# Kernel tuning notes

Hardware: AMD Instinct MI355X
Metric: run time of the kernel (lower is better)

## Reference

```python
import jax, jax.numpy as jnp
import numpy as np

B, T, D, H, STEPS = 4096, 128, 4, 64, 60


def setup_inputs() -> dict:
    key = jax.random.key(0)
    ks = jax.random.split(key, 12)
    s = 0.1
    return {
        "x": jax.random.normal(ks[0], (B, T, D), dtype=jnp.float32),
        # layer 0 (input size D)
        "Wih0": jax.random.normal(ks[1], (4 * H, D), dtype=jnp.float32) * s,
        "Whh0": jax.random.normal(ks[2], (4 * H, H), dtype=jnp.float32) * s,
        "bih0": jax.random.normal(ks[3], (4 * H,), dtype=jnp.float32) * s,
        "bhh0": jax.random.normal(ks[4], (4 * H,), dtype=jnp.float32) * s,
        # layer 1 (input size H)
        "Wih1": jax.random.normal(ks[5], (4 * H, H), dtype=jnp.float32) * s,
        "Whh1": jax.random.normal(ks[6], (4 * H, H), dtype=jnp.float32) * s,
        "bih1": jax.random.normal(ks[7], (4 * H,), dtype=jnp.float32) * s,
        "bhh1": jax.random.normal(ks[8], (4 * H,), dtype=jnp.float32) * s,
        # output head
        "Wfc": jax.random.normal(ks[9], (D, H), dtype=jnp.float32) * s,
        "bfc": jax.random.normal(ks[10], (D,), dtype=jnp.float32) * s,
    }


def _lstm_cell(h, c, x, Wih, Whh, bih, bhh):
    # PyTorch gate order: i, f, g, o
    gates = x @ Wih.T + h @ Whh.T + (bih + bhh)  # [B, 4H]
    i, f, g, o = jnp.split(gates, 4, axis=-1)
    c_new = jax.nn.sigmoid(f) * c + jax.nn.sigmoid(i) * jnp.tanh(g)
    h_new = jax.nn.sigmoid(o) * jnp.tanh(c_new)
    return h_new, c_new


def reference(x, Wih0, Whh0, bih0, bhh0, Wih1, Whh1, bih1, bhh1, Wfc, bfc):
    b = x.shape[0]
    zeros = jnp.zeros((b, H), dtype=x.dtype)

    def two_layer(carry, xt):
        h0, c0, h1, c1 = carry
        h0, c0 = _lstm_cell(h0, c0, xt, Wih0, Whh0, bih0, bhh0)
        h1, c1 = _lstm_cell(h1, c1, h0, Wih1, Whh1, bih1, bhh1)
        return (h0, c0, h1, c1), h1

    # encode history: scan over time (xs: [T, B, D])
    carry0 = (zeros, zeros, zeros, zeros)
    carry, _ = jax.lax.scan(two_layer, carry0, jnp.swapaxes(x, 0, 1))

    def ar_step(state, _):
        carry, cur = state
        carry, h1 = two_layer(carry, cur)
        pred = h1 @ Wfc.T + bfc  # [B, D]
        return (carry, pred), pred

    _, preds = jax.lax.scan(ar_step, (carry, x[:, -1, :]), None, length=STEPS)
    return jnp.swapaxes(preds, 0, 1)  # [B, STEPS, D]
```

## Files before the change

kernel.cpp:

```cpp
#include <hip/hip_runtime.h>


#define T_ENC 128
#define D_IN 4
#define H 64
#define STEPS 60
#define M 16
#define A0S 104
#define A1S 136

typedef _Float16 half8 __attribute__((ext_vector_type(8)));
typedef _Float16 half4_t __attribute__((ext_vector_type(4)));
typedef float float4v __attribute__((ext_vector_type(4)));

__device__ __forceinline__ float fast_sigmoid(float x) {
    float e = __builtin_amdgcn_exp2f(-1.44269504f * x);
    return __builtin_amdgcn_rcpf(1.0f + e);
}
__device__ __forceinline__ float fast_tanh(float x) {
    float e = __builtin_amdgcn_exp2f(2.88539008f * x);
    return __builtin_fmaf(-2.0f, __builtin_amdgcn_rcpf(e + 1.0f), 1.0f);
}

__global__ __launch_bounds__(256, 1) void lstm_ar_kernel(
    const float* __restrict__ x,
    const float* __restrict__ Wih0, const float* __restrict__ Whh0,
    const float* __restrict__ bih0, const float* __restrict__ bhh0,
    const float* __restrict__ Wih1, const float* __restrict__ Whh1,
    const float* __restrict__ bih1, const float* __restrict__ bhh1,
    const float* __restrict__ Wfc,  const float* __restrict__ bfc,
    float* __restrict__ out)
{
    __shared__ __align__(16) _Float16 A0buf[2][M * A0S];
    __shared__ __align__(16) _Float16 A1buf[2][M * A1S];
    __shared__ __align__(16) float    xstash[2][512];
    __shared__ __align__(16) float    predsS[M * STEPS * D_IN];

    const int tid  = threadIdx.x;
    const int wave = tid >> 6;
    const int lane = tid & 63;
    const int n16  = lane & 15;
    const int quad = lane >> 4;
    const int m0   = blockIdx.x * M;
    const int m    = n16;
    const int jcol = 16 * wave + n16;

    { _Float16* z = &A0buf[0][0]; for (int i = tid; i < 2 * M * A0S; i += 256) z[i] = (_Float16)0.f; }
    { _Float16* z = &A1buf[0][0]; for (int i = tid; i < 2 * M * A1S; i += 256) z[i] = (_Float16)0.f; }

    half8 B0f[3][4];
    half8 B1f[4][4];
    half8 B0ar[4][4];
    half8 Bfc[2];
    float b0v[4], b1v[4], b0ar[4];
    #pragma unroll
    for (int tau = 0; tau < 4; ++tau) {
        const int n = 16 * (wave + 4 * tau) + n16;
        b0v[tau] = bih0[n] + bhh0[n];
        b1v[tau] = bih1[n] + bhh1[n];
        float wb = 0.f;
        #pragma unroll
        for (int d = 0; d < 4; ++d) wb += Wih0[n * D_IN + d] * bfc[d];
        b0ar[tau] = b0v[tau] + wb;
        #pragma unroll
        for (int kt = 0; kt < 3; ++kt)
            #pragma unroll
            for (int j = 0; j < 8; ++j) {
                const int k = kt * 32 + quad * 8 + j;
                float v = 0.f;
                if (k < 4)       v = Wih0[n * D_IN + k];
                else if (k < 68) v = Whh0[n * H + (k - 4)];
                B0f[kt][tau][j] = (_Float16)v;
            }
        #pragma unroll
        for (int kt = 0; kt < 4; ++kt)
            #pragma unroll
            for (int j = 0; j < 8; ++j) {
                const int k = kt * 32 + quad * 8 + j;
                const float v = (k < H) ? Wih1[n * H + k] : Whh1[n * H + (k - H)];
                B1f[kt][tau][j] = (_Float16)v;
            }
        #pragma unroll
        for (int kt = 0; kt < 4; ++kt)
            #pragma unroll
            for (int j = 0; j < 8; ++j) {
                const int k = kt * 32 + quad * 8 + j;
                float v;
                if (k < H) v = Whh0[n * H + k];
                else {
                    const int c = k - H;
                    v = Wih0[n * D_IN + 0] * Wfc[0 * H + c] + Wih0[n * D_IN + 1] * Wfc[1 * H + c]
                      + Wih0[n * D_IN + 2] * Wfc[2 * H + c] + Wih0[n * D_IN + 3] * Wfc[3 * H + c];
                }
                B0ar[kt][tau][j] = (_Float16)v;
            }
    }
    float bfcv = 0.f;
    if (wave == 0) {
        #pragma unroll
        for (int kt = 0; kt < 2; ++kt)
            #pragma unroll
            for (int j = 0; j < 8; ++j) {
                const int k = kt * 32 + quad * 8 + j;
                Bfc[kt][j] = (_Float16)((n16 < 4) ? Wfc[n16 * H + k] : 0.f);
            }
        if (n16 < 4) bfcv = bfc[n16];
    }

    float c0s[4] = {0.f, 0.f, 0.f, 0.f};
    float c1s[4] = {0.f, 0.f, 0.f, 0.f};

    __syncthreads();

    if (wave == 2) {
        const int elem = lane >> 2, st2 = (lane & 3) * 2;
        const float4v xa = *(const float4v*)&x[((size_t)(m0 + elem) * T_ENC + st2) * 4];
        const float4v xb = *(const float4v*)&x[((size_t)(m0 + elem) * T_ENC + st2 + 1) * 4];
        *(float4v*)&xstash[0][elem * 32 + st2 * 4]       = xa;
        *(float4v*)&xstash[0][elem * 32 + (st2 + 1) * 4] = xb;
    }
    __syncthreads();
    if (wave == 2 && lane < 16) {
        const float4v v0 = *(const float4v*)&xstash[0][lane * 32 + 0];
        const float4v v1 = *(const float4v*)&xstash[0][lane * 32 + 4];
        *(half4_t*)&A0buf[1][lane * A0S] =
            (half4_t){(_Float16)v0[0], (_Float16)v0[1], (_Float16)v0[2], (_Float16)v0[3]};
        *(half4_t*)&A0buf[0][lane * A0S] =
            (half4_t){(_Float16)v1[0], (_Float16)v1[1], (_Float16)v1[2], (_Float16)v1[3]};
    }
    __syncthreads();

    {
        half8 a0f[3];
        #pragma unroll
        for (int kt = 0; kt < 3; ++kt)
            a0f[kt] = *(const half8*)&A0buf[1][m * A0S + kt * 32 + quad * 8];
        float4v C0[4];
        #pragma unroll
        for (int tau = 0; tau < 4; ++tau)
            C0[tau] = (float4v){b0v[tau], b0v[tau], b0v[tau], b0v[tau]};
        #pragma unroll
        for (int kt = 0; kt < 3; ++kt)
            #pragma unroll
            for (int tau = 0; tau < 4; ++tau)
                C0[tau] = __builtin_amdgcn_mfma_f32_16x16x32_f16(a0f[kt], B0f[kt][tau], C0[tau], 0, 0, 0);
        #pragma unroll
        for (int r = 0; r < 4; ++r) {
            const float ig = fast_sigmoid(C0[0][r]);
            const float fg = fast_sigmoid(C0[1][r]);
            const float gg = fast_tanh   (C0[2][r]);
            const float og = fast_sigmoid(C0[3][r]);
            const float c  = fg * c0s[r] + ig * gg;
            c0s[r] = c;
            const _Float16 hh = (_Float16)(og * fast_tanh(c));
            const int row = quad * 4 + r;
            A1buf[0][row * A1S + jcol]     = hh;
            A0buf[0][row * A0S + 4 + jcol] = hh;
        }
    }
    __syncthreads();

    float4v xpa, xpb;

    for (int t = 0; t < T_ENC; ++t) {
        const int p = t & 1;
        const _Float16* cur0 = &A0buf[p][0];
        const _Float16* cur1 = &A1buf[p][0];
        _Float16* nxt0 = &A0buf[1 - p][0];
        _Float16* nxt1 = &A1buf[1 - p][0];

        if (wave == 2) {
            if ((t & 7) == 0) {
                const int k = (t >> 3) + 1;
                const int elem = lane >> 2, st2 = (lane & 3) * 2;
                int t1 = 8 * k + st2;     if (t1 > 127) t1 = 127;
                int t2 = 8 * k + st2 + 1; if (t2 > 127) t2 = 127;
                xpa = *(const float4v*)&x[((size_t)(m0 + elem) * T_ENC + t1) * 4];
                xpb = *(const float4v*)&x[((size_t)(m0 + elem) * T_ENC + t2) * 4];
            }
            if ((t & 7) == 4) {
                const int bf = ((t >> 3) + 1) & 1;
                const int elem = lane >> 2, st2 = (lane & 3) * 2;
                *(float4v*)&xstash[bf][elem * 32 + st2 * 4]       = xpa;
                *(float4v*)&xstash[bf][elem * 32 + (st2 + 1) * 4] = xpb;
            }
        }

        half8 a1f[4], a0f[3];
        #pragma unroll
        for (int kt = 0; kt < 4; ++kt)
            a1f[kt] = *(const half8*)&cur1[m * A1S + kt * 32 + quad * 8];
        #pragma unroll
        for (int kt = 0; kt < 3; ++kt)
            a0f[kt] = *(const half8*)&cur0[m * A0S + kt * 32 + quad * 8];

        float4v C1[4], C0[4];
        #pragma unroll
        for (int tau = 0; tau < 4; ++tau) {
            C1[tau] = (float4v){b1v[tau], b1v[tau], b1v[tau], b1v[tau]};
            C0[tau] = (float4v){b0v[tau], b0v[tau], b0v[tau], b0v[tau]};
        }
        #pragma unroll
        for (int kt = 0; kt < 4; ++kt)
            #pragma unroll
            for (int tau = 0; tau < 4; ++tau)
                C1[tau] = __builtin_amdgcn_mfma_f32_16x16x32_f16(a1f[kt], B1f[kt][tau], C1[tau], 0, 0, 0);
        #pragma unroll
        for (int kt = 0; kt < 3; ++kt)
            #pragma unroll
            for (int tau = 0; tau < 4; ++tau)
                C0[tau] = __builtin_amdgcn_mfma_f32_16x16x32_f16(a0f[kt], B0f[kt][tau], C0[tau], 0, 0, 0);

        #pragma unroll
        for (int r = 0; r < 4; ++r) {
            const float ig = fast_sigmoid(C1[0][r]);
            const float fg = fast_sigmoid(C1[1][r]);
            const float gg = fast_tanh   (C1[2][r]);
            const float og = fast_sigmoid(C1[3][r]);
            const float c  = fg * c1s[r] + ig * gg;
            c1s[r] = c;
            const int row = quad * 4 + r;
            nxt1[row * A1S + 64 + jcol] = (_Float16)(og * fast_tanh(c));
        }
        #pragma unroll
        for (int r = 0; r < 4; ++r) {
            const float ig = fast_sigmoid(C0[0][r]);
            const float fg = fast_sigmoid(C0[1][r]);
            const float gg = fast_tanh   (C0[2][r]);
            const float og = fast_sigmoid(C0[3][r]);
            const float c  = fg * c0s[r] + ig * gg;
            c0s[r] = c;
            const _Float16 hh = (_Float16)(og * fast_tanh(c));
            const int row = quad * 4 + r;
            nxt1[row * A1S + jcol]     = hh;
            nxt0[row * A0S + 4 + jcol] = hh;
        }
        if (wave == 2 && lane < 16) {
            const int st = (t + 2) & 7, bf = ((t + 2) >> 3) & 1;
            const float4v v = *(const float4v*)&xstash[bf][lane * 32 + st * 4];
            *(half4_t*)&nxt0[lane * A0S] =
                (half4_t){(_Float16)v[0], (_Float16)v[1], (_Float16)v[2], (_Float16)v[3]};
        }
        __syncthreads();
    }

    for (int s = 0; s < STEPS; ++s) {
        const int q = s & 1;
        const _Float16* cur = &A1buf[q][0];
        _Float16* nxt = &A1buf[1 - q][0];

        half8 a1f[4];
        #pragma unroll
        for (int kt = 0; kt < 4; ++kt)
            a1f[kt] = *(const half8*)&cur[m * A1S + kt * 32 + quad * 8];
        float4v C1[4];
        #pragma unroll
        for (int tau = 0; tau < 4; ++tau)
            C1[tau] = (float4v){b1v[tau], b1v[tau], b1v[tau], b1v[tau]};
        #pragma unroll
        for (int kt = 0; kt < 4; ++kt)
            #pragma unroll
            for (int tau = 0; tau < 4; ++tau)
                C1[tau] = __builtin_amdgcn_mfma_f32_16x16x32_f16(a1f[kt], B1f[kt][tau], C1[tau], 0, 0, 0);
        #pragma unroll
        for (int r = 0; r < 4; ++r) {
            const float ig = fast_sigmoid(C1[0][r]);
            const float fg = fast_sigmoid(C1[1][r]);
            const float gg = fast_tanh   (C1[2][r]);
            const float og = fast_sigmoid(C1[3][r]);
            const float c  = fg * c1s[r] + ig * gg;
            c1s[r] = c;
            const int row = quad * 4 + r;
            nxt[row * A1S + 64 + jcol] = (_Float16)(og * fast_tanh(c));
        }
        __syncthreads();

        half8 aA[4];
        #pragma unroll
        for (int kt = 0; kt < 2; ++kt)
            aA[kt] = *(const half8*)&cur[m * A1S + kt * 32 + quad * 8];
        #pragma unroll
        for (int kt = 2; kt < 4; ++kt)
            aA[kt] = *(const half8*)&nxt[m * A1S + 64 + (kt - 2) * 32 + quad * 8];
        float4v C0[4];
        #pragma unroll
        for (int tau = 0; tau < 4; ++tau)
            C0[tau] = (float4v){b0ar[tau], b0ar[tau], b0ar[tau], b0ar[tau]};
        #pragma unroll
        for (int kt = 0; kt < 4; ++kt)
            #pragma unroll
            for (int tau = 0; tau < 4; ++tau)
                C0[tau] = __builtin_amdgcn_mfma_f32_16x16x32_f16(aA[kt], B0ar[kt][tau], C0[tau], 0, 0, 0);

        if (wave == 0) {
            float4v Cp = (float4v){bfcv, bfcv, bfcv, bfcv};
            Cp = __builtin_amdgcn_mfma_f32_16x16x32_f16(aA[2], Bfc[0], Cp, 0, 0, 0);
            Cp = __builtin_amdgcn_mfma_f32_16x16x32_f16(aA[3], Bfc[1], Cp, 0, 0, 0);
            if (n16 < 4) {
                #pragma unroll
                for (int r = 0; r < 4; ++r)
                    predsS[(quad * 4 + r) * (STEPS * D_IN) + s * 4 + n16] = Cp[r];
            }
        }

        #pragma unroll
        for (int r = 0; r < 4; ++r) {
            const float ig = fast_sigmoid(C0[0][r]);
            const float fg = fast_sigmoid(C0[1][r]);
            const float gg = fast_tanh   (C0[2][r]);
            const float og = fast_sigmoid(C0[3][r]);
            const float c  = fg * c0s[r] + ig * gg;
            c0s[r] = c;
            const int row = quad * 4 + r;
            nxt[row * A1S + jcol] = (_Float16)(og * fast_tanh(c));
        }
        __syncthreads();
    }

    for (int j = tid; j < M * STEPS; j += 256) {
        const int elem = j / STEPS, r = j - elem * STEPS;
        ((float4v*)out)[(size_t)(m0 + elem) * STEPS + r] = ((const float4v*)predsS)[j];
    }
}

extern "C" void kernel_launch(void* const* d_in, const int* in_sizes, int n_in,
                              void* d_out, int out_size, void* d_ws, size_t ws_size,
                              hipStream_t stream) {
    const float* x    = (const float*)d_in[0];
    const float* Wih0 = (const float*)d_in[1];
    const float* Whh0 = (const float*)d_in[2];
    const float* bih0 = (const float*)d_in[3];
    const float* bhh0 = (const float*)d_in[4];
    const float* Wih1 = (const float*)d_in[5];
    const float* Whh1 = (const float*)d_in[6];
    const float* bih1 = (const float*)d_in[7];
    const float* bhh1 = (const float*)d_in[8];
    const float* Wfc  = (const float*)d_in[9];
    const float* bfc  = (const float*)d_in[10];
    float* out = (float*)d_out;

    dim3 grid(4096 / M);
    dim3 block(256);
    lstm_ar_kernel<<<grid, block, 0, stream>>>(
        x, Wih0, Whh0, bih0, bhh0, Wih1, Whh1, bih1, bhh1, Wfc, bfc, out);
}
```

Baseline: 308.2 us.

## Split LSTM layers across two wave groups with 512-thread blocks

Doubles the block to 512 threads so one group of four waves runs layer 1 while the other runs layer 0, in parallel within each timestep. The whole x tile is preloaded once into shared memory as fp16 instead of being streamed through a double-buffered float stash. In the rollout, each group precomputes the partial MFMA products it can already form before the barrier, which shortens the work after each sync. This removes the serial layer-0/layer-1 work per wave. In exchange it needs more LDS and registers per block, and the launch bound now asks for two blocks per CU.

New measurement: 261.8 us. 1.18x faster.

```diff
diff --git a/kernel.cpp b/kernel.cpp
--- a/kernel.cpp
+++ b/kernel.cpp
@@ -8,6 +8,7 @@
 #define M 16
 #define A0S 104
 #define A1S 136
+#define XN (M * T_ENC * D_IN)
 
 typedef _Float16 half8 __attribute__((ext_vector_type(8)));
 typedef _Float16 half4_t __attribute__((ext_vector_type(4)));
@@ -22,7 +23,7 @@
     return __builtin_fmaf(-2.0f, __builtin_amdgcn_rcpf(e + 1.0f), 1.0f);
 }
 
-__global__ __launch_bounds__(256, 1) void lstm_ar_kernel(
+__global__ __launch_bounds__(512, 2) void lstm_ar_kernel(
     const float* __restrict__ x,
     const float* __restrict__ Wih0, const float* __restrict__ Whh0,
     const float* __restrict__ bih0, const float* __restrict__ bhh0,
@@ -33,7 +34,7 @@
 {
     __shared__ __align__(16) _Float16 A0buf[2][M * A0S];
     __shared__ __align__(16) _Float16 A1buf[2][M * A1S];
-    __shared__ __align__(16) float    xstash[2][512];
+    __shared__ __align__(16) _Float16 xAll[XN];
     __shared__ __align__(16) float    predsS[M * STEPS * D_IN];
 
     const int tid  = threadIdx.x;
@@ -41,70 +42,56 @@
     const int lane = tid & 63;
     const int n16  = lane & 15;
     const int quad = lane >> 4;
+    const int grp  = wave >> 2;
+    const int w4   = wave & 3;
     const int m0   = blockIdx.x * M;
     const int m    = n16;
-    const int jcol = 16 * wave + n16;
-
-    { _Float16* z = &A0buf[0][0]; for (int i = tid; i < 2 * M * A0S; i += 256) z[i] = (_Float16)0.f; }
-    { _Float16* z = &A1buf[0][0]; for (int i = tid; i < 2 * M * A1S; i += 256) z[i] = (_Float16)0.f; }
-
+    const int jcol = 16 * w4 + n16;
+
+    { _Float16* z = &A0buf[0][0]; for (int i = tid; i < 2 * M * A0S; i += 512) z[i] = (_Float16)0.f; }
+    { _Float16* z = &A1buf[0][0]; for (int i = tid; i < 2 * M * A1S; i += 512) z[i] = (_Float16)0.f; }
+    for (int j = tid; j < XN / 4; j += 512) {
+        const float4v v = *(const float4v*)&x[(size_t)m0 * T_ENC * D_IN + (size_t)j * 4];
+        *(half4_t*)&xAll[j * 4] =
+            (half4_t){(_Float16)v[0], (_Float16)v[1], (_Float16)v[2], (_Float16)v[3]};
+    }
+
+    half8 B1f[4][4];
     half8 B0f[3][4];
-    half8 B1f[4][4];
-    half8 B0ar[4][4];
-    half8 Bfc[2];
-    float b0v[4], b1v[4], b0ar[4];
-    #pragma unroll
-    for (int tau = 0; tau < 4; ++tau) {
-        const int n = 16 * (wave + 4 * tau) + n16;
-        b0v[tau] = bih0[n] + bhh0[n];
-        b1v[tau] = bih1[n] + bhh1[n];
-        float wb = 0.f;
-        #pragma unroll
-        for (int d = 0; d < 4; ++d) wb += Wih0[n * D_IN + d] * bfc[d];
-        b0ar[tau] = b0v[tau] + wb;
-        #pragma unroll
-        for (int kt = 0; kt < 3; ++kt)
-            #pragma unroll
-            for (int j = 0; j < 8; ++j) {
-                const int k = kt * 32 + quad * 8 + j;
-                float v = 0.f;
-                if (k < 4)       v = Wih0[n * D_IN + k];
-                else if (k < 68) v = Whh0[n * H + (k - 4)];
-                B0f[kt][tau][j] = (_Float16)v;
-            }
-        #pragma unroll
-        for (int kt = 0; kt < 4; ++kt)
-            #pragma unroll
-            for (int j = 0; j < 8; ++j) {
-                const int k = kt * 32 + quad * 8 + j;
-                const float v = (k < H) ? Wih1[n * H + k] : Whh1[n * H + (k - H)];
-                B1f[kt][tau][j] = (_Float16)v;
-            }
-        #pragma unroll
-        for (int kt = 0; kt < 4; ++kt)
-            #pragma unroll
-            for (int j = 0; j < 8; ++j) {
-                const int k = kt * 32 + quad * 8 + j;
-                float v;
-                if (k < H) v = Whh0[n * H + k];
-                else {
-                    const int c = k - H;
-                    v = Wih0[n * D_IN + 0] * Wfc[0 * H + c] + Wih0[n * D_IN + 1] * Wfc[1 * H + c]
-                      + Wih0[n * D_IN + 2] * Wfc[2 * H + c] + Wih0[n * D_IN + 3] * Wfc[3 * H + c];
-                }
-                B0ar[kt][tau][j] = (_Float16)v;
-            }
-    }
-    float bfcv = 0.f;
-    if (wave == 0) {
-        #pragma unroll
-        for (int kt = 0; kt < 2; ++kt)
-            #pragma unroll
-            for (int j = 0; j < 8; ++j) {
-                const int k = kt * 32 + quad * 8 + j;
-                Bfc[kt][j] = (_Float16)((n16 < 4) ? Wfc[n16 * H + k] : 0.f);
-            }
-        if (n16 < 4) bfcv = bfc[n16];
+    float b1v[4], b0v[4], b0arv[4];
+    if (grp == 0) {
+        #pragma unroll
+        for (int tau = 0; tau < 4; ++tau) {
+            const int n = 16 * (w4 + 4 * tau) + n16;
+            b1v[tau] = bih1[n] + bhh1[n];
+            #pragma unroll
+            for (int kt = 0; kt < 4; ++kt)
+                #pragma unroll
+                for (int j = 0; j < 8; ++j) {
+                    const int k = kt * 32 + quad * 8 + j;
+                    B1f[kt][tau][j] = (_Float16)((k < H) ? Wih1[n * H + k] : Whh1[n * H + (k - H)]);
+                }
+        }
+    } else {
+        #pragma unroll
+        for (int tau = 0; tau < 4; ++tau) {
+            const int n = 16 * (w4 + 4 * tau) + n16;
+            b0v[tau] = bih0[n] + bhh0[n];
+            float wb = 0.f;
+            #pragma unroll
+            for (int d = 0; d < 4; ++d) wb += Wih0[n * D_IN + d] * bfc[d];
+            b0arv[tau] = b0v[tau] + wb;
+            #pragma unroll
+            for (int kt = 0; kt < 3; ++kt)
+                #pragma unroll
+                for (int j = 0; j < 8; ++j) {
+                    const int k = kt * 32 + quad * 8 + j;
+                    float v = 0.f;
+                    if (k < 4)       v = Wih0[n * D_IN + k];
+                    else if (k < 68) v = Whh0[n * H + (k - 4)];
+                    B0f[kt][tau][j] = (_Float16)v;
+                }
+        }
     }
 
     float c0s[4] = {0.f, 0.f, 0.f, 0.f};
@@ -112,25 +99,13 @@
 
     __syncthreads();
 
-    if (wave == 2) {
-        const int elem = lane >> 2, st2 = (lane & 3) * 2;
-        const float4v xa = *(const float4v*)&x[((size_t)(m0 + elem) * T_ENC + st2) * 4];
-        const float4v xb = *(const float4v*)&x[((size_t)(m0 + elem) * T_ENC + st2 + 1) * 4];
-        *(float4v*)&xstash[0][elem * 32 + st2 * 4]       = xa;
-        *(float4v*)&xstash[0][elem * 32 + (st2 + 1) * 4] = xb;
+    if (grp == 1 && w4 == 2 && lane < 16) {
+        *(half4_t*)&A0buf[1][lane * A0S] = *(const half4_t*)&xAll[(lane * T_ENC + 0) * D_IN];
+        *(half4_t*)&A0buf[0][lane * A0S] = *(const half4_t*)&xAll[(lane * T_ENC + 1) * D_IN];
     }
     __syncthreads();
-    if (wave == 2 && lane < 16) {
-        const float4v v0 = *(const float4v*)&xstash[0][lane * 32 + 0];
-        const float4v v1 = *(const float4v*)&xstash[0][lane * 32 + 4];
-        *(half4_t*)&A0buf[1][lane * A0S] =
-            (half4_t){(_Float16)v0[0], (_Float16)v0[1], (_Float16)v0[2], (_Float16)v0[3]};
-        *(half4_t*)&A0buf[0][lane * A0S] =
-            (half4_t){(_Float16)v1[0], (_Float16)v1[1], (_Float16)v1[2], (_Float16)v1[3]};
-    }
-    __syncthreads();
-
-    {
+
+    if (grp == 1) {
         half8 a0f[3];
         #pragma unroll
         for (int kt = 0; kt < 3; ++kt)
@@ -160,88 +135,119 @@
     }
     __syncthreads();
 
-    float4v xpa, xpb;
-
     for (int t = 0; t < T_ENC; ++t) {
         const int p = t & 1;
-        const _Float16* cur0 = &A0buf[p][0];
-        const _Float16* cur1 = &A1buf[p][0];
-        _Float16* nxt0 = &A0buf[1 - p][0];
-        _Float16* nxt1 = &A1buf[1 - p][0];
-
-        if (wave == 2) {
-            if ((t & 7) == 0) {
-                const int k = (t >> 3) + 1;
-                const int elem = lane >> 2, st2 = (lane & 3) * 2;
-                int t1 = 8 * k + st2;     if (t1 > 127) t1 = 127;
-                int t2 = 8 * k + st2 + 1; if (t2 > 127) t2 = 127;
-                xpa = *(const float4v*)&x[((size_t)(m0 + elem) * T_ENC + t1) * 4];
-                xpb = *(const float4v*)&x[((size_t)(m0 + elem) * T_ENC + t2) * 4];
-            }
-            if ((t & 7) == 4) {
-                const int bf = ((t >> 3) + 1) & 1;
-                const int elem = lane >> 2, st2 = (lane & 3) * 2;
-                *(float4v*)&xstash[bf][elem * 32 + st2 * 4]       = xpa;
-                *(float4v*)&xstash[bf][elem * 32 + (st2 + 1) * 4] = xpb;
-            }
-        }
-
-        half8 a1f[4], a0f[3];
-        #pragma unroll
-        for (int kt = 0; kt < 4; ++kt)
-            a1f[kt] = *(const half8*)&cur1[m * A1S + kt * 32 + quad * 8];
-        #pragma unroll
-        for (int kt = 0; kt < 3; ++kt)
-            a0f[kt] = *(const half8*)&cur0[m * A0S + kt * 32 + quad * 8];
-
-        float4v C1[4], C0[4];
+        if (grp == 0) {
+            const _Float16* cur1 = &A1buf[p][0];
+            _Float16* nxt1 = &A1buf[1 - p][0];
+            half8 a1f[4];
+            #pragma unroll
+            for (int kt = 0; kt < 4; ++kt)
+                a1f[kt] = *(const half8*)&cur1[m * A1S + kt * 32 + quad * 8];
+            float4v C1[4];
+            #pragma unroll
+            for (int tau = 0; tau < 4; ++tau)
+                C1[tau] = (float4v){b1v[tau], b1v[tau], b1v[tau], b1v[tau]};
+            #pragma unroll
+            for (int kt = 0; kt < 4; ++kt)
+                #pragma unroll
+                for (int tau = 0; tau < 4; ++tau)
+                    C1[tau] = __builtin_amdgcn_mfma_f32_16x16x32_f16(a1f[kt], B1f[kt][tau], C1[tau], 0, 0, 0);
+            #pragma unroll
+            for (int r = 0; r < 4; ++r) {
+                const float ig = fast_sigmoid(C1[0][r]);
+                const float fg = fast_sigmoid(C1[1][r]);
+                const float gg = fast_tanh   (C1[2][r]);
+                const float og = fast_sigmoid(C1[3][r]);
+                const float c  = fg * c1s[r] + ig * gg;
+                c1s[r] = c;
+                nxt1[(quad * 4 + r) * A1S + 64 + jcol] = (_Float16)(og * fast_tanh(c));
+            }
+        } else {
+            const _Float16* cur0 = &A0buf[p][0];
+            _Float16* nxt0 = &A0buf[1 - p][0];
+            _Float16* nxt1 = &A1buf[1 - p][0];
+            half8 a0f[3];
+            #pragma unroll
+            for (int kt = 0; kt < 3; ++kt)
+                a0f[kt] = *(const half8*)&cur0[m * A0S + kt * 32 + quad * 8];
+            float4v C0[4];
+            #pragma unroll
+            for (int tau = 0; tau < 4; ++tau)
+                C0[tau] = (float4v){b0v[tau], b0v[tau], b0v[tau], b0v[tau]};
+            #pragma unroll
+            for (int kt = 0; kt < 3; ++kt)
+                #pragma unroll
+                for (int tau = 0; tau < 4; ++tau)
+                    C0[tau] = __builtin_amdgcn_mfma_f32_16x16x32_f16(a0f[kt], B0f[kt][tau], C0[tau], 0, 0, 0);
+            #pragma unroll
+            for (int r = 0; r < 4; ++r) {
+                const float ig = fast_sigmoid(C0[0][r]);
+                const float fg = fast_sigmoid(C0[1][r]);
+                const float gg = fast_tanh   (C0[2][r]);
+                const float og = fast_sigmoid(C0[3][r]);
+                const float c  = fg * c0s[r] + ig * gg;
+                c0s[r] = c;
+                const _Float16 hh = (_Float16)(og * fast_tanh(c));
+                const int row = quad * 4 + r;
+                nxt1[row * A1S + jcol]     = hh;
+                nxt0[row * A0S + 4 + jcol] = hh;
+            }
+            if (w4 == 2 && lane < 16) {
+                int tn = t + 2; if (tn > T_ENC - 1) tn = T_ENC - 1;
+                *(half4_t*)&nxt0[lane * A0S] = *(const half4_t*)&xAll[(lane * T_ENC + tn) * D_IN];
+            }
+        }
+        __syncthreads();
+    }
+
+    half8 B0ar[4][4];
+    half8 Bfc[2];
+    float bfcv = 0.f;
+    if (grp == 1) {
         #pragma unroll
         for (int tau = 0; tau < 4; ++tau) {
-            C1[tau] = (float4v){b1v[tau], b1v[tau], b1v[tau], b1v[tau]};
-            C0[tau] = (float4v){b0v[tau], b0v[tau], b0v[tau], b0v[tau]};
-        }
-        #pragma unroll
-        for (int kt = 0; kt < 4; ++kt)
-            #pragma unroll
-            for (int tau = 0; tau < 4; ++tau)
-                C1[tau] = __builtin_amdgcn_mfma_f32_16x16x32_f16(a1f[kt], B1f[kt][tau], C1[tau], 0, 0, 0);
-        #pragma unroll
-        for (int kt = 0; kt < 3; ++kt)
-            #pragma unroll
-            for (int tau = 0; tau < 4; ++tau)
-                C0[tau] = __builtin_amdgcn_mfma_f32_16x16x32_f16(a0f[kt], B0f[kt][tau], C0[tau], 0, 0, 0);
-
-        #pragma unroll
-        for (int r = 0; r < 4; ++r) {
-            const float ig = fast_sigmoid(C1[0][r]);
-            const float fg = fast_sigmoid(C1[1][r]);
-            const float gg = fast_tanh   (C1[2][r]);
-            const float og = fast_sigmoid(C1[3][r]);
-            const float c  = fg * c1s[r] + ig * gg;
-            c1s[r] = c;
-            const int row = quad * 4 + r;
-            nxt1[row * A1S + 64 + jcol] = (_Float16)(og * fast_tanh(c));
-        }
-        #pragma unroll
-        for (int r = 0; r < 4; ++r) {
-            const float ig = fast_sigmoid(C0[0][r]);
-            const float fg = fast_sigmoid(C0[1][r]);
-            const float gg = fast_tanh   (C0[2][r]);
-            const float og = fast_sigmoid(C0[3][r]);
-            const float c  = fg * c0s[r] + ig * gg;
-            c0s[r] = c;
-            const _Float16 hh = (_Float16)(og * fast_tanh(c));
-            const int row = quad * 4 + r;
-            nxt1[row * A1S + jcol]     = hh;
-            nxt0[row * A0S + 4 + jcol] = hh;
-        }
-        if (wave == 2 && lane < 16) {
-            const int st = (t + 2) & 7, bf = ((t + 2) >> 3) & 1;
-            const float4v v = *(const float4v*)&xstash[bf][lane * 32 + st * 4];
-            *(half4_t*)&nxt0[lane * A0S] =
-                (half4_t){(_Float16)v[0], (_Float16)v[1], (_Float16)v[2], (_Float16)v[3]};
-        }
-        __syncthreads();
+            const int n = 16 * (w4 + 4 * tau) + n16;
+            #pragma unroll
+            for (int kt = 0; kt < 4; ++kt)
+                #pragma unroll
+                for (int j = 0; j < 8; ++j) {
+                    const int k = kt * 32 + quad * 8 + j;
+                    float v;
+                    if (k < H) v = Whh0[n * H + k];
+                    else {
+                        const int c = k - H;
+                        v = Wih0[n * D_IN + 0] * Wfc[0 * H + c] + Wih0[n * D_IN + 1] * Wfc[1 * H + c]
+                          + Wih0[n * D_IN + 2] * Wfc[2 * H + c] + Wih0[n * D_IN + 3] * Wfc[3 * H + c];
+                    }
+                    B0ar[kt][tau][j] = (_Float16)v;
+                }
+        }
+        if (w4 == 0) {
+            #pragma unroll
+            for (int kt = 0; kt < 2; ++kt)
+                #pragma unroll
+                for (int j = 0; j < 8; ++j) {
+                    const int k = kt * 32 + quad * 8 + j;
+                    Bfc[kt][j] = (_Float16)((n16 < 4) ? Wfc[n16 * H + k] : 0.f);
+                }
+            if (n16 < 4) bfcv = bfc[n16];
+        }
+    }
+    float4v C1pre[4];
+    if (grp == 0) {
+        half8 ah[2];
+        #pragma unroll
+        for (int kt = 0; kt < 2; ++kt)
+            ah[kt] = *(const half8*)&A1buf[0][m * A1S + 64 + kt * 32 + quad * 8];
+        #pragma unroll
+        for (int tau = 0; tau < 4; ++tau)
+            C1pre[tau] = (float4v){b1v[tau], b1v[tau], b1v[tau], b1v[tau]};
+        #pragma unroll
+        for (int kt = 0; kt < 2; ++kt)
+            #pragma unroll
+            for (int tau = 0; tau < 4; ++tau)
+                C1pre[tau] = __builtin_amdgcn_mfma_f32_16x16x32_f16(ah[kt], B1f[2 + kt][tau], C1pre[tau], 0, 0, 0);
     }
 
     for (int s = 0; s < STEPS; ++s) {
@@ -249,75 +255,87 @@
         const _Float16* cur = &A1buf[q][0];
         _Float16* nxt = &A1buf[1 - q][0];
 
-        half8 a1f[4];
-        #pragma unroll
-        for (int kt = 0; kt < 4; ++kt)
-            a1f[kt] = *(const half8*)&cur[m * A1S + kt * 32 + quad * 8];
-        float4v C1[4];
-        #pragma unroll
-        for (int tau = 0; tau < 4; ++tau)
-            C1[tau] = (float4v){b1v[tau], b1v[tau], b1v[tau], b1v[tau]};
-        #pragma unroll
-        for (int kt = 0; kt < 4; ++kt)
-            #pragma unroll
-            for (int tau = 0; tau < 4; ++tau)
-                C1[tau] = __builtin_amdgcn_mfma_f32_16x16x32_f16(a1f[kt], B1f[kt][tau], C1[tau], 0, 0, 0);
-        #pragma unroll
-        for (int r = 0; r < 4; ++r) {
-            const float ig = fast_sigmoid(C1[0][r]);
-            const float fg = fast_sigmoid(C1[1][r]);
-            const float gg = fast_tanh   (C1[2][r]);
-            const float og = fast_sigmoid(C1[3][r]);
-            const float c  = fg * c1s[r] + ig * gg;
-            c1s[r] = c;
-            const int row = quad * 4 + r;
-            nxt[row * A1S + 64 + jcol] = (_Float16)(og * fast_tanh(c));
+        half8 ah0[2];
+        #pragma unroll
+        for (int kt = 0; kt < 2; ++kt)
+            ah0[kt] = *(const half8*)&cur[m * A1S + kt * 32 + quad * 8];
+
+        float4v C0pre[4];
+        if (grp == 0) {
+            float4v C1[4] = {C1pre[0], C1pre[1], C1pre[2], C1pre[3]};
+            #pragma unroll
+            for (int kt = 0; kt < 2; ++kt)
+                #pragma unroll
+                for (int tau = 0; tau < 4; ++tau)
+                    C1[tau] = __builtin_amdgcn_mfma_f32_16x16x32_f16(ah0[kt], B1f[kt][tau], C1[tau], 0, 0, 0);
+            #pragma unroll
+            for (int r = 0; r < 4; ++r) {
+                const float ig = fast_sigmoid(C1[0][r]);
+                const float fg = fast_sigmoid(C1[1][r]);
+                const float gg = fast_tanh   (C1[2][r]);
+                const float og = fast_sigmoid(C1[3][r]);
+                const float c  = fg * c1s[r] + ig * gg;
+                c1s[r] = c;
+                nxt[(quad * 4 + r) * A1S + 64 + jcol] = (_Float16)(og * fast_tanh(c));
+            }
+        } else {
+            #pragma unroll
+            for (int tau = 0; tau < 4; ++tau)
+                C0pre[tau] = (float4v){b0arv[tau], b0arv[tau], b0arv[tau], b0arv[tau]};
+            #pragma unroll
+            for (int kt = 0; kt < 2; ++kt)
+                #pragma unroll
+                for (int tau = 0; tau < 4; ++tau)
+                    C0pre[tau] = __builtin_amdgcn_mfma_f32_16x16x32_f16(ah0[kt], B0ar[kt][tau], C0pre[tau], 0, 0, 0);
         }
         __syncthreads();
 
-        half8 aA[4];
+        half8 ah1[2];
         #pragma unroll
         for (int kt = 0; kt < 2; ++kt)
-            aA[kt] = *(const half8*)&cur[m * A1S + kt * 32 + quad * 8];
-        #pragma unroll
-        for (int kt = 2; kt < 4; ++kt)
-            aA[kt] = *(const half8*)&nxt[m * A1S + 64 + (kt - 2) * 32 + quad * 8];
-        float4v C0[4];
-        #pragma unroll
-        for (int tau = 0; tau < 4; ++tau)
-            C0[tau] = (float4v){b0ar[tau], b0ar[tau], b0ar[tau], b0ar[tau]};
-        #pragma unroll
-        for (int kt = 0; kt < 4; ++kt)
-            #pragma unroll
-            for (int tau = 0; tau < 4; ++tau)
-                C0[tau] = __builtin_amdgcn_mfma_f32_16x16x32_f16(aA[kt], B0ar[kt][tau], C0[tau], 0, 0, 0);
-
-        if (wave == 0) {
-            float4v Cp = (float4v){bfcv, bfcv, bfcv, bfcv};
-            Cp = __builtin_amdgcn_mfma_f32_16x16x32_f16(aA[2], Bfc[0], Cp, 0, 0, 0);
-            Cp = __builtin_amdgcn_mfma_f32_16x16x32_f16(aA[3], Bfc[1], Cp, 0, 0, 0);
-            if (n16 < 4) {
-                #pragma unroll
-                for (int r = 0; r < 4; ++r)
-                    predsS[(quad * 4 + r) * (STEPS * D_IN) + s * 4 + n16] = Cp[r];
-            }
-        }
-
-        #pragma unroll
-        for (int r = 0; r < 4; ++r) {
-            const float ig = fast_sigmoid(C0[0][r]);
-            const float fg = fast_sigmoid(C0[1][r]);
-            const float gg = fast_tanh   (C0[2][r]);
-            const float og = fast_sigmoid(C0[3][r]);
-            const float c  = fg * c0s[r] + ig * gg;
-            c0s[r] = c;
-            const int row = quad * 4 + r;
-            nxt[row * A1S + jcol] = (_Float16)(og * fast_tanh(c));
+            ah1[kt] = *(const half8*)&nxt[m * A1S + 64 + kt * 32 + quad * 8];
+
+        if (grp == 1) {
+            float4v C0[4] = {C0pre[0], C0pre[1], C0pre[2], C0pre[3]};
+            #pragma unroll
+            for (int kt = 0; kt < 2; ++kt)
+                #pragma unroll
+                for (int tau = 0; tau < 4; ++tau)
+                    C0[tau] = __builtin_amdgcn_mfma_f32_16x16x32_f16(ah1[kt], B0ar[2 + kt][tau], C0[tau], 0, 0, 0);
+            if (w4 == 0) {
+                float4v Cp = (float4v){bfcv, bfcv, bfcv, bfcv};
+                Cp = __builtin_amdgcn_mfma_f32_16x16x32_f16(ah1[0], Bfc[0], Cp, 0, 0, 0);
+                Cp = __builtin_amdgcn_mfma_f32_16x16x32_f16(ah1[1], Bfc[1], Cp, 0, 0, 0);
+                if (n16 < 4) {
+                    #pragma unroll
+                    for (int r = 0; r < 4; ++r)
+                        predsS[(quad * 4 + r) * (STEPS * D_IN) + s * D_IN + n16] = Cp[r];
+                }
+            }
+            #pragma unroll
+            for (int r = 0; r < 4; ++r) {
+                const float ig = fast_sigmoid(C0[0][r]);
+                const float fg = fast_sigmoid(C0[1][r]);
+                const float gg = fast_tanh   (C0[2][r]);
+                const float og = fast_sigmoid(C0[3][r]);
+                const float c  = fg * c0s[r] + ig * gg;
+                c0s[r] = c;
+                nxt[(quad * 4 + r) * A1S + jcol] = (_Float16)(og * fast_tanh(c));
+            }
+        } else {
+            #pragma unroll
+            for (int tau = 0; tau < 4; ++tau)
+                C1pre[tau] = (float4v){b1v[tau], b1v[tau], b1v[tau], b1v[tau]};
+            #pragma unroll
+            for (int kt = 0; kt < 2; ++kt)
+                #pragma unroll
+                for (int tau = 0; tau < 4; ++tau)
+                    C1pre[tau] = __builtin_amdgcn_mfma_f32_16x16x32_f16(ah1[kt], B1f[2 + kt][tau], C1pre[tau], 0, 0, 0);
         }
         __syncthreads();
     }
 
-    for (int j = tid; j < M * STEPS; j += 256) {
+    for (int j = tid; j < M * STEPS; j += 512) {
         const int elem = j / STEPS, r = j - elem * STEPS;
         ((float4v*)out)[(size_t)(m0 + elem) * STEPS + r] = ((const float4v*)predsS)[j];
     }
@@ -340,7 +358,7 @@
     float* out = (float*)d_out;
 
     dim3 grid(4096 / M);
-    dim3 block(256);
+    dim3 block(512);
     lstm_ar_kernel<<<grid, block, 0, stream>>>(
         x, Wih0, Whh0, bih0, bhh0, Wih1, Whh1, bih1, bhh1, Wfc, bfc, out);
 }
```
